# Performance work log

Hardware: AMD Instinct MI355X
Metric: run time of the kernel (lower is better)

Reference implementation:

```python
import jax, jax.numpy as jnp
import numpy as np

B, T, V, E, H, L = 64, 512, 100, 100, 256, 8


def _lstm_layer(xs, w_ih, w_hh, b_ih, b_hh):
    # xs: [B, T, I]; PyTorch gate order: i, f, g, o
    gx = jnp.einsum('bti,gi->btg', xs, w_ih) + b_ih  # [B, T, 4H]
    gx = jnp.swapaxes(gx, 0, 1)                      # [T, B, 4H]
    w_hh_t = w_hh.T                                  # [H, 4H]
    h0 = jnp.zeros((xs.shape[0], w_hh.shape[1]), xs.dtype)

    def step(carry, g):
        h, c = carry
        g = g + h @ w_hh_t + b_hh
        i, f, gg, o = jnp.split(g, 4, axis=-1)
        c = jax.nn.sigmoid(f) * c + jax.nn.sigmoid(i) * jnp.tanh(gg)
        h = jax.nn.sigmoid(o) * jnp.tanh(c)
        return (h, c), h

    (hT, cT), ys = jax.lax.scan(step, (h0, h0), gx)
    return jnp.swapaxes(ys, 0, 1), hT, cT


def setup_inputs() -> dict:
    key = jax.random.key(0)
    ks = jax.random.split(key, 9)
    s = 0.05  # roughly PyTorch's 1/sqrt(H) uniform scale
    return {
        'x': jax.random.randint(ks[0], (B, T), 0, V),
        'embed': jax.random.normal(ks[1], (V, E), jnp.float32) * s,
        'w_ih0': jax.random.normal(ks[2], (4 * H, E), jnp.float32) * s,
        'w_ih': jax.random.normal(ks[3], (L - 1, 4 * H, H), jnp.float32) * s,
        'w_hh': jax.random.normal(ks[4], (L, 4 * H, H), jnp.float32) * s,
        'b_ih': jax.random.normal(ks[5], (L, 4 * H), jnp.float32) * s,
        'b_hh': jax.random.normal(ks[6], (L, 4 * H), jnp.float32) * s,
        'fc_w': jax.random.normal(ks[7], (V, H), jnp.float32) * s,
        'fc_b': jax.random.normal(ks[8], (V,), jnp.float32) * s,
    }


def reference(x, embed, w_ih0, w_ih, w_hh, b_ih, b_hh, fc_w, fc_b):
    h = embed[x]  # [B, T, E]
    h_fin, c_fin = [], []
    for l in range(L):
        wih = w_ih0 if l == 0 else w_ih[l - 1]
        h, hT, cT = _lstm_layer(h, wih, w_hh[l], b_ih[l], b_hh[l])
        h_fin.append(hT)
        c_fin.append(cT)
    logits = jnp.einsum('bth,vh->btv', h, fc_w) + fc_b  # [B, T, V]
    return logits, jnp.stack(h_fin), jnp.stack(c_fin)
```

## Files before the change

### kernel.cpp

```cpp
#include <hip/hip_runtime.h>


typedef _Float16 f16;
typedef f16  f16x8 __attribute__((ext_vector_type(8)));
typedef f16  f16x4 __attribute__((ext_vector_type(4)));
typedef float f32x4 __attribute__((ext_vector_type(4)));
typedef int   i32x4 __attribute__((ext_vector_type(4)));

#define DEV __device__ __forceinline__

constexpr int TT = 512, BB = 64, VV = 100, HH = 256, LL = 8;
constexpr int RING_D = 32;
constexpr int POISON = 0x7C007C00;
constexpr int MAXRETRY = 4096;

constexpr size_t XE_OFF = 0;
constexpr size_t XE_SZ  = (size_t)TT*BB*256*2;
constexpr size_t WP_OFF = XE_OFF + XE_SZ;
constexpr size_t WP_SZ  = (size_t)LL*16*64*512*2;
constexpr size_t BI_OFF = WP_OFF + WP_SZ;
constexpr size_t BI_SZ  = (size_t)LL*16*64*4;
constexpr size_t FW_OFF = BI_OFF + BI_SZ;
constexpr size_t FW_SZ  = (size_t)112*256*2;
constexpr size_t H7_OFF = FW_OFF + FW_SZ;
constexpr size_t H7_SZ  = (size_t)TT*BB*256*2;
constexpr size_t HR_OFF = H7_OFF + H7_SZ;
constexpr size_t HR_SZ  = (size_t)LL*RING_D*BB*256*2;
constexpr size_t XR_OFF = HR_OFF + HR_SZ;
constexpr size_t XR_SZ  = (size_t)7*RING_D*BB*256*2;
constexpr size_t FCF_OFF = XR_OFF + XR_SZ;
constexpr size_t FCF_SZ  = (size_t)7*TT*16;
constexpr size_t XC_OFF  = FCF_OFF + FCF_SZ;
constexpr size_t XC_SZ   = 128;
constexpr int ZERO_DW = (int)((FCF_SZ + XC_SZ) / 4);
constexpr int POIS_TH = (int)((HR_SZ + XR_SZ) / 16);

DEV void ld16_pl (i32x4& d, const void* p){ asm volatile("global_load_dwordx4 %0, %1, off"     : "=v"(d) : "v"(p)); }
DEV void ld16_sc0(i32x4& d, const void* p){ asm volatile("global_load_dwordx4 %0, %1, off sc0" : "=v"(d) : "v"(p)); }
DEV void ld16_sc1(i32x4& d, const void* p){ asm volatile("global_load_dwordx4 %0, %1, off sc1" : "=v"(d) : "v"(p)); }
DEV void st16_sc0(void* p, i32x4 d){ asm volatile("global_store_dwordx4 %0, %1, off sc0" :: "v"(p), "v"(d) : "memory"); }
DEV void st16_sc1(void* p, i32x4 d){ asm volatile("global_store_dwordx4 %0, %1, off sc1" :: "v"(p), "v"(d) : "memory"); }
DEV void stb_sc1(void* p){ unsigned o = 1; asm volatile("global_store_byte %0, %1, off sc1" :: "v"(p), "v"(o) : "memory"); }
DEV void stb_val_sc1(void* p, unsigned v){ asm volatile("global_store_byte %0, %1, off sc1" :: "v"(p), "v"(v) : "memory"); }
DEV void wait_vm0(){ asm volatile("s_waitcnt vmcnt(0)" ::: "memory"); __builtin_amdgcn_sched_barrier(0); }
DEV void wait_vm8(){ asm volatile("s_waitcnt vmcnt(8)" ::: "memory"); __builtin_amdgcn_sched_barrier(0); }

DEV bool chk8(const i32x4* f) {
  int bad = 0;
  #pragma unroll
  for (int i = 0; i < 8; ++i) {
    bad |= (f[i][0] == POISON);
    bad |= (f[i][1] == POISON);
    bad |= (f[i][2] == POISON);
    bad |= (f[i][3] == POISON);
  }
  return __all(bad == 0);
}

DEV bool poll16(const unsigned char* p) {
  for (int it = 0; it < (1 << 16); ++it) {
    i32x4 f;
    asm volatile("global_load_dwordx4 %0, %1, off sc1\n\ts_waitcnt vmcnt(0)"
                 : "=v"(f) : "v"(p) : "memory");
    if ((f[0] & f[1] & f[2] & f[3]) == 0x01010101) return true;
    if (it > 2) __builtin_amdgcn_s_sleep(1);
  }
  return false;
}

DEV bool hs_poll(const unsigned char* p) {
  for (int it = 0; it < (1 << 20); ++it) {
    i32x4 f;
    asm volatile("global_load_dwordx4 %0, %1, off sc1\n\ts_waitcnt vmcnt(0)"
                 : "=v"(f) : "v"(p) : "memory");
    int a = f[0] & f[1] & f[2] & f[3];
    if ((a & 0x10101010) == 0x10101010) {
      int e = (f[0] & 0xFF) * 0x01010101;
      return f[0] == e && f[1] == e && f[2] == e && f[3] == e;
    }
    __builtin_amdgcn_s_sleep(1);
  }
  return false;
}

DEV float sig2(float y)  { return __builtin_amdgcn_rcpf(1.f + __builtin_amdgcn_exp2f(-y)); }
DEV float tanhp(float y) { return 1.f - 2.f * __builtin_amdgcn_rcpf(1.f + __builtin_amdgcn_exp2f(y)); }
constexpr float LOG2E = 1.4426950408889634f;
constexpr float C2LE  = 2.8853900817779268f;
DEV unsigned f16bits(float v) { f16 h = (f16)v; return (unsigned)__builtin_bit_cast(unsigned short, h); }

__global__ void prep_zero(unsigned int* p, int n) {
  int i = blockIdx.x * 256 + threadIdx.x;
  if (i < n) p[i] = 0;
}
__global__ void prep_poison(unsigned int* p) {
  size_t i = ((size_t)blockIdx.x * 256 + threadIdx.x) * 4;
  i32x4 P = {POISON, POISON, POISON, POISON};
  *(i32x4*)(p + i) = P;
}

__global__ void prep_embed(const int* __restrict__ x, const float* __restrict__ em,
                           f16* __restrict__ xe) {
  int g = blockIdx.x * 256 + threadIdx.x;
  int chunk = g & 7, pair = g >> 3;
  int b = pair & 63, t = pair >> 6;
  int idx = x[b * 512 + t];
  const float* er = em + (size_t)idx * 100;
  f16* o = xe + (size_t)pair * 256 + chunk * 32;
  #pragma unroll
  for (int c4 = 0; c4 < 32; c4 += 4) {
    f16x4 v;
    #pragma unroll
    for (int q = 0; q < 4; ++q) {
      int c = chunk * 32 + c4 + q;
      v[q] = (c < 100) ? (f16)er[c] : (f16)0.f;
    }
    *(f16x4*)(o + c4) = v;
  }
}

__global__ void prep_w(const float* __restrict__ w_ih0, const float* __restrict__ w_ih,
                       const float* __restrict__ w_hh, f16* __restrict__ wpo) {
  int g = blockIdx.x * 256 + threadIdx.x;
  int k4 = (g & 127) * 4;
  int n  = (g >> 7) & 63;
  int ls = g >> 13;
  int l = ls >> 4, s = ls & 15;
  int gate = n & 3;
  int u = s * 16 + ((n >> 4) << 2) + ((n >> 2) & 3);
  int r = 256 * gate + u;
  float scale = (gate == 2) ? C2LE : LOG2E;
  f16x4 v;
  #pragma unroll
  for (int q = 0; q < 4; ++q) {
    int k = k4 + q;
    float f;
    if (k < 256) {
      if (l == 0) f = (k < 100) ? w_ih0[(size_t)r * 100 + k] : 0.f;
      else        f = w_ih[((size_t)(l - 1) * 1024 + r) * 256 + k];
    } else        f = w_hh[((size_t)l * 1024 + r) * 256 + (k - 256)];
    v[q] = (f16)(f * scale);
  }
  *(f16x4*)(wpo + (size_t)g * 4) = v;
}

__global__ void prep_bias(const float* __restrict__ b_ih, const float* __restrict__ b_hh,
                          float* __restrict__ bo) {
  int g = blockIdx.x * 256 + threadIdx.x;
  int n = g & 63, s = (g >> 6) & 15, l = g >> 10;
  int gate = n & 3;
  int u = s * 16 + ((n >> 4) << 2) + ((n >> 2) & 3);
  int r = 256 * gate + u;
  float scale = (gate == 2) ? C2LE : LOG2E;
  bo[g] = (b_ih[l * 1024 + r] + b_hh[l * 1024 + r]) * scale;
}

__global__ void prep_fcw(const float* __restrict__ fc_w, f16* __restrict__ fo) {
  int g = blockIdx.x * 256 + threadIdx.x;
  int n = g >> 6, k4 = (g & 63) * 4;
  f16x4 v;
  #pragma unroll
  for (int q = 0; q < 4; ++q)
    v[q] = (n < 100) ? (f16)fc_w[(size_t)n * 256 + k4 + q] : (f16)0.f;
  *(f16x4*)(fo + (size_t)g * 4) = v;
}

__global__ void __launch_bounds__(512, 1) lstm_pipe(
    const f16* __restrict__ xe, const f16* __restrict__ wp, const float* __restrict__ biasp,
    f16* h7, f16* hrg, f16* xrg, unsigned char* fcf, unsigned char* xc, float* out)
{
  __shared__ char pad_lds[40960];
  __shared__ unsigned short pub[2][64][24];
  (void)((volatile char*)pad_lds)[threadIdx.x];

  const int bx  = blockIdx.x;
  const int lyr = bx & 7;
  const int sl  = bx >> 3;
  const int tid = threadIdx.x;
  const int wv  = tid >> 6;
  const int ln  = tid & 63;
  const int mA  = wv >> 2;
  const int nB  = wv & 3;

  f16x8 wfa[2][16];
  {
    const f16* wb = wp + (size_t)(lyr * 16 + sl) * 64 * 512;
    #pragma unroll
    for (int tt = 0; tt < 2; ++tt)
      #pragma unroll
      for (int kt = 0; kt < 16; ++kt) {
        wfa[tt][kt] = *(const f16x8*)(wb + (size_t)((2 * mA + tt) * 16 + (ln & 15)) * 512
                                      + kt * 32 + (ln >> 4) * 8);
        i32x4 pin = __builtin_bit_cast(i32x4, wfa[tt][kt]);
        asm volatile("" : "+v"(pin));
        wfa[tt][kt] = __builtin_bit_cast(f16x8, pin);
      }
  }
  f32x4 bias_v[2];
  #pragma unroll
  for (int tt = 0; tt < 2; ++tt) {
    bias_v[tt] = *(const f32x4*)(biasp + (size_t)(lyr * 16 + sl) * 64
                                 + (2 * mA + tt) * 16 + (ln >> 4) * 4);
    asm volatile("" : "+v"(bias_v[tt]));
  }

  unsigned xcc = 0;
  asm volatile("s_getreg_b32 %0, hwreg(20, 0, 32)" : "=s"(xcc));
  unsigned char* xcg = xc + lyr * 16;
  if (tid == 0) stb_val_sc1(xcg + sl, 0x10 | (xcc & 15));
  const bool fast = hs_poll(xcg);

  float cst0 = 0.f, cst1 = 0.f;
  const int q    = ln >> 4;
  const int bcol = nB * 16 + (ln & 15);
  const int kof  = q * 8;
  const f16* xring = xrg + (size_t)(lyr - 1) * RING_D * 16384;
  f16*       xdst  = xrg + (size_t)lyr * RING_D * 16384;
  f16*       hring = hrg + (size_t)lyr * RING_D * 16384;
  bool dead = false;

  for (int t = 0; t < TT; ++t) {
    if (wv == 0 && t + 1 < TT) {
      if (lyr < 7 && t + 1 >= RING_D && !dead)
        dead = !poll16(fcf + (size_t)(lyr * TT + (t + 1 - RING_D)) * 16);
      i32x4 P = {POISON, POISON, POISON, POISON};
      f16* pz = hring + (size_t)((t + 1) & (RING_D - 1)) * 16384
              + (size_t)ln * 256 + sl * 16;
      if (fast) { st16_sc0(pz, P); st16_sc0(pz + 8, P); }
      else      { st16_sc1(pz, P); st16_sc1(pz + 8, P); }
      if (lyr < 7) {
        f16* px = xdst + (size_t)((t + 1) & (RING_D - 1)) * 16384
                + (size_t)ln * 256 + sl * 16;
        st16_sc1(px, P);
        st16_sc1(px + 8, P);
      }
    }

    const bool hasH = (t > 0);
    i32x4 bfx[8], bfh[8];
    {
      const f16* xb = ((lyr == 0) ? xe + (size_t)t * 16384
                                  : xring + (size_t)(t & (RING_D - 1)) * 16384)
                      + (size_t)bcol * 256 + kof;
      if (lyr == 0) {
        #pragma unroll
        for (int kt = 0; kt < 8; ++kt) ld16_pl(bfx[kt], xb + kt * 32);
      } else {
        #pragma unroll
        for (int kt = 0; kt < 8; ++kt) ld16_sc1(bfx[kt], xb + kt * 32);
      }
      if (hasH) {
        const f16* hb = hring + (size_t)((t - 1) & (RING_D - 1)) * 16384
                      + (size_t)bcol * 256 + kof;
        if (fast) {
          #pragma unroll
          for (int kt = 0; kt < 8; ++kt) ld16_sc0(bfh[kt], hb + kt * 32);
        } else {
          #pragma unroll
          for (int kt = 0; kt < 8; ++kt) ld16_sc1(bfh[kt], hb + kt * 32);
        }
      }
    }
    if (hasH) wait_vm8(); else wait_vm0();

    if (lyr > 0 && !dead) {
      int it = 0;
      while (!chk8(bfx)) {
        if (++it > MAXRETRY) { dead = true; break; }
        wait_vm0();
        const f16* xb = xring + (size_t)(t & (RING_D - 1)) * 16384
                      + (size_t)bcol * 256 + kof;
        #pragma unroll
        for (int kt = 0; kt < 8; ++kt) ld16_sc1(bfx[kt], xb + kt * 32);
        wait_vm0();
      }
    }

    f32x4 acc0 = {0,0,0,0}, acc1 = {0,0,0,0};
    #pragma unroll
    for (int kt = 0; kt < 8; ++kt) {
      f16x8 av = __builtin_bit_cast(f16x8, bfx[kt]);
      acc0 = __builtin_amdgcn_mfma_f32_16x16x32_f16(wfa[0][kt], av, acc0, 0, 0, 0);
      acc1 = __builtin_amdgcn_mfma_f32_16x16x32_f16(wfa[1][kt], av, acc1, 0, 0, 0);
    }

    if (hasH) {
      wait_vm0();
      if (!dead) {
        int it = 0;
        while (!chk8(bfh)) {
          if (++it > MAXRETRY) { dead = true; break; }
          const f16* hb = hring + (size_t)((t - 1) & (RING_D - 1)) * 16384
                        + (size_t)bcol * 256 + kof;
          if (fast) {
            #pragma unroll
            for (int kt = 0; kt < 8; ++kt) ld16_sc0(bfh[kt], hb + kt * 32);
          } else {
            #pragma unroll
            for (int kt = 0; kt < 8; ++kt) ld16_sc1(bfh[kt], hb + kt * 32);
          }
          wait_vm0();
        }
      }
      #pragma unroll
      for (int kt = 0; kt < 8; ++kt) {
        f16x8 av = __builtin_bit_cast(f16x8, bfh[kt]);
        acc0 = __builtin_amdgcn_mfma_f32_16x16x32_f16(wfa[0][8 + kt], av, acc0, 0, 0, 0);
        acc1 = __builtin_amdgcn_mfma_f32_16x16x32_f16(wfa[1][8 + kt], av, acc1, 0, 0, 0);
      }
    }

    const int par = t & 1;
    #pragma unroll
    for (int tt = 0; tt < 2; ++tt) {
      f32x4 g4 = (tt == 0 ? acc0 : acc1);
      g4 += bias_v[tt];
      float i_ = sig2(g4[0]), f_ = sig2(g4[1]), z_ = tanhp(g4[2]), o_ = sig2(g4[3]);
      float& c_ = (tt == 0 ? cst0 : cst1);
      c_ = f_ * c_ + i_ * z_;
      float h_ = o_ * tanhp(c_ * C2LE);
      pub[par][bcol][(2 * mA + tt) * 4 + q] = (unsigned short)f16bits(h_);
      if (t == TT - 1) {
        const int u = sl * 16 + (2 * mA + tt) * 4 + q;
        size_t ob = 3276800 + (size_t)lyr * 16384 + (size_t)bcol * 256 + u;
        out[ob] = h_;  out[ob + 131072] = c_;
      }
    }
    __syncthreads();

    if (wv == 0) {
      i32x4 d0 = *(const i32x4*)&pub[par][ln][0];
      i32x4 d1 = *(const i32x4*)&pub[par][ln][8];
      f16* hd = hring + (size_t)(t & (RING_D - 1)) * 16384 + (size_t)ln * 256 + sl * 16;
      if (fast) { st16_sc0(hd, d0); st16_sc0(hd + 8, d1); }
      else      { st16_sc1(hd, d0); st16_sc1(hd + 8, d1); }
      if (lyr < 7) {
        f16* xd = xdst + (size_t)(t & (RING_D - 1)) * 16384 + (size_t)ln * 256 + sl * 16;
        st16_sc1(xd, d0);
        st16_sc1(xd + 8, d1);
      } else {
        f16* h7d = h7 + (size_t)t * 16384 + (size_t)ln * 256 + sl * 16;
        *(i32x4*)h7d = d0;
        *(i32x4*)(h7d + 8) = d1;
      }
      if (ln == 1 && lyr > 0)
        stb_sc1(fcf + (size_t)((lyr - 1) * TT + t) * 16 + sl);
    }
  }
}

__global__ void __launch_bounds__(256, 1) fc_kernel(
    const f16* __restrict__ h7, const f16* __restrict__ fcw,
    const float* __restrict__ fcb, float* __restrict__ out)
{
  const int t  = blockIdx.x;
  const int wv = threadIdx.x >> 6;
  const int ln = threadIdx.x & 63;
  const f16* ab = h7 + (size_t)t * 16384 + (size_t)(wv * 16 + (ln & 15)) * 256 + (ln >> 4) * 8;
  f16x8 af[8];
  #pragma unroll
  for (int kt = 0; kt < 8; ++kt) af[kt] = *(const f16x8*)(ab + kt * 32);
  const int obrow = wv * 16 + (ln >> 4) * 4;
  #pragma unroll
  for (int nt = 0; nt < 7; ++nt) {
    const f16* bb = fcw + (size_t)(nt * 16 + (ln & 15)) * 256 + (ln >> 4) * 8;
    f32x4 acc = {0, 0, 0, 0};
    #pragma unroll
    for (int kt = 0; kt < 8; ++kt) {
      f16x8 bv = *(const f16x8*)(bb + kt * 32);
      acc = __builtin_amdgcn_mfma_f32_16x16x32_f16(af[kt], bv, acc, 0, 0, 0);
    }
    int vg = nt * 16 + (ln & 15);
    if (vg < VV) {
      float bias = fcb[vg];
      #pragma unroll
      for (int j = 0; j < 4; ++j)
        out[(size_t)(obrow + j) * 51200 + (size_t)t * 100 + vg] = acc[j] + bias;
    }
  }
}

extern "C" void kernel_launch(void* const* d_in, const int* in_sizes, int n_in,
                              void* d_out, int out_size, void* d_ws, size_t ws_size,
                              hipStream_t stream) {
  (void)in_sizes; (void)n_in; (void)out_size; (void)ws_size;
  const int*   x     = (const int*)d_in[0];
  const float* embed = (const float*)d_in[1];
  const float* w_ih0 = (const float*)d_in[2];
  const float* w_ih  = (const float*)d_in[3];
  const float* w_hh  = (const float*)d_in[4];
  const float* b_ih  = (const float*)d_in[5];
  const float* b_hh  = (const float*)d_in[6];
  const float* fc_w  = (const float*)d_in[7];
  const float* fc_b  = (const float*)d_in[8];
  char* ws = (char*)d_ws;
  float* out = (float*)d_out;

  prep_zero<<<57, 256, 0, stream>>>((unsigned int*)(ws + FCF_OFF), ZERO_DW);
  prep_poison<<<POIS_TH / 256, 256, 0, stream>>>((unsigned int*)(ws + HR_OFF));
  prep_embed<<<1024, 256, 0, stream>>>(x, embed, (f16*)(ws + XE_OFF));
  prep_w<<<4096, 256, 0, stream>>>(w_ih0, w_ih, w_hh, (f16*)(ws + WP_OFF));
  prep_bias<<<32, 256, 0, stream>>>(b_ih, b_hh, (float*)(ws + BI_OFF));
  prep_fcw<<<28, 256, 0, stream>>>(fc_w, (f16*)(ws + FW_OFF));

  lstm_pipe<<<128, 512, 35072, stream>>>(
      (const f16*)(ws + XE_OFF), (const f16*)(ws + WP_OFF), (const float*)(ws + BI_OFF),
      (f16*)(ws + H7_OFF), (f16*)(ws + HR_OFF), (f16*)(ws + XR_OFF),
      (unsigned char*)(ws + FCF_OFF), (unsigned char*)(ws + XC_OFF), out);

  fc_kernel<<<512, 256, 0, stream>>>((const f16*)(ws + H7_OFF), (const f16*)(ws + FW_OFF),
                                     fc_b, out);
}
```

Before: 3.215 ms.

## Software-pipeline input projection one timestep ahead of recurrent step in LSTM pipe

```diff
diff --git a/kernel.cpp b/kernel.cpp
--- a/kernel.cpp
+++ b/kernel.cpp
@@ -33,7 +33,7 @@
 constexpr size_t XC_OFF  = FCF_OFF + FCF_SZ;
 constexpr size_t XC_SZ   = 128;
 constexpr int ZERO_DW = (int)((FCF_SZ + XC_SZ) / 4);
-constexpr int POIS_TH = (int)((HR_SZ + XR_SZ) / 16);
+constexpr int POIS_BLK = (int)((HR_SZ + XR_SZ) / 16 / 256);
 
 DEV void ld16_pl (i32x4& d, const void* p){ asm volatile("global_load_dwordx4 %0, %1, off"     : "=v"(d) : "v"(p)); }
 DEV void ld16_sc0(i32x4& d, const void* p){ asm volatile("global_load_dwordx4 %0, %1, off sc0" : "=v"(d) : "v"(p)); }
@@ -219,73 +219,55 @@
   f16*       hring = hrg + (size_t)lyr * RING_D * 16384;
   bool dead = false;
 
-  for (int t = 0; t < TT; ++t) {
-    if (wv == 0 && t + 1 < TT) {
-      if (lyr < 7 && t + 1 >= RING_D && !dead)
-        dead = !poll16(fcf + (size_t)(lyr * TT + (t + 1 - RING_D)) * 16);
-      i32x4 P = {POISON, POISON, POISON, POISON};
-      f16* pz = hring + (size_t)((t + 1) & (RING_D - 1)) * 16384
-              + (size_t)ln * 256 + sl * 16;
-      if (fast) { st16_sc0(pz, P); st16_sc0(pz + 8, P); }
-      else      { st16_sc1(pz, P); st16_sc1(pz + 8, P); }
-      if (lyr < 7) {
-        f16* px = xdst + (size_t)((t + 1) & (RING_D - 1)) * 16384
-                + (size_t)ln * 256 + sl * 16;
-        st16_sc1(px, P);
-        st16_sc1(px + 8, P);
-      }
-    }
-
-    const bool hasH = (t > 0);
-    i32x4 bfx[8], bfh[8];
-    {
-      const f16* xb = ((lyr == 0) ? xe + (size_t)t * 16384
-                                  : xring + (size_t)(t & (RING_D - 1)) * 16384)
-                      + (size_t)bcol * 256 + kof;
-      if (lyr == 0) {
-        #pragma unroll
-        for (int kt = 0; kt < 8; ++kt) ld16_pl(bfx[kt], xb + kt * 32);
-      } else {
-        #pragma unroll
-        for (int kt = 0; kt < 8; ++kt) ld16_sc1(bfx[kt], xb + kt * 32);
-      }
-      if (hasH) {
-        const f16* hb = hring + (size_t)((t - 1) & (RING_D - 1)) * 16384
-                      + (size_t)bcol * 256 + kof;
-        if (fast) {
-          #pragma unroll
-          for (int kt = 0; kt < 8; ++kt) ld16_sc0(bfh[kt], hb + kt * 32);
-        } else {
-          #pragma unroll
-          for (int kt = 0; kt < 8; ++kt) ld16_sc1(bfh[kt], hb + kt * 32);
-        }
-      }
-    }
-    if (hasH) wait_vm8(); else wait_vm0();
-
-    if (lyr > 0 && !dead) {
+  i32x4 bfx[8], bfh[8];
+  f32x4 aX0 = {0,0,0,0}, aX1 = {0,0,0,0};
+
+  {
+    const f16* xb = ((lyr == 0) ? xe : xring) + (size_t)bcol * 256 + kof;
+    if (lyr == 0) { 
+      #pragma unroll
+      for (int kt = 0; kt < 8; ++kt) ld16_pl(bfx[kt], xb + kt * 32);
+    } else {
+      #pragma unroll
+      for (int kt = 0; kt < 8; ++kt) ld16_sc1(bfx[kt], xb + kt * 32);
+    }
+    wait_vm0();
+    if (lyr > 0) {
       int it = 0;
       while (!chk8(bfx)) {
         if (++it > MAXRETRY) { dead = true; break; }
-        wait_vm0();
-        const f16* xb = xring + (size_t)(t & (RING_D - 1)) * 16384
-                      + (size_t)bcol * 256 + kof;
         #pragma unroll
         for (int kt = 0; kt < 8; ++kt) ld16_sc1(bfx[kt], xb + kt * 32);
         wait_vm0();
       }
     }
-
-    f32x4 acc0 = {0,0,0,0}, acc1 = {0,0,0,0};
     #pragma unroll
     for (int kt = 0; kt < 8; ++kt) {
       f16x8 av = __builtin_bit_cast(f16x8, bfx[kt]);
-      acc0 = __builtin_amdgcn_mfma_f32_16x16x32_f16(wfa[0][kt], av, acc0, 0, 0, 0);
-      acc1 = __builtin_amdgcn_mfma_f32_16x16x32_f16(wfa[1][kt], av, acc1, 0, 0, 0);
-    }
-
+      aX0 = __builtin_amdgcn_mfma_f32_16x16x32_f16(wfa[0][kt], av, aX0, 0, 0, 0);
+      aX1 = __builtin_amdgcn_mfma_f32_16x16x32_f16(wfa[1][kt], av, aX1, 0, 0, 0);
+    }
+    if (lyr > 0 && wv == 0 && ln == 1)
+      stb_sc1(fcf + (size_t)((lyr - 1) * TT + 0) * 16 + sl);
+    const f16* xb1 = ((lyr == 0) ? xe + 16384 : xring + 16384)
+                     + (size_t)bcol * 256 + kof;
+    if (lyr == 0) {
+      #pragma unroll
+      for (int kt = 0; kt < 8; ++kt) ld16_pl(bfx[kt], xb1 + kt * 32);
+    } else {
+      #pragma unroll
+      for (int kt = 0; kt < 8; ++kt) ld16_sc1(bfx[kt], xb1 + kt * 32);
+    }
+  }
+
+  for (int t = 0; t < TT; ++t) {
+    const bool hasH  = (t > 0);
+    const bool lastT = (t == TT - 1);
+
+    wait_vm8();
+
+    f32x4 a0 = aX0, a1 = aX1;
     if (hasH) {
-      wait_vm0();
       if (!dead) {
         int it = 0;
         while (!chk8(bfh)) {
@@ -305,25 +287,67 @@
       #pragma unroll
       for (int kt = 0; kt < 8; ++kt) {
         f16x8 av = __builtin_bit_cast(f16x8, bfh[kt]);
-        acc0 = __builtin_amdgcn_mfma_f32_16x16x32_f16(wfa[0][8 + kt], av, acc0, 0, 0, 0);
-        acc1 = __builtin_amdgcn_mfma_f32_16x16x32_f16(wfa[1][8 + kt], av, acc1, 0, 0, 0);
+        a0 = __builtin_amdgcn_mfma_f32_16x16x32_f16(wfa[0][8 + kt], av, a0, 0, 0, 0);
+        a1 = __builtin_amdgcn_mfma_f32_16x16x32_f16(wfa[1][8 + kt], av, a1, 0, 0, 0);
+      }
+    }
+
+    if (!lastT) {
+      wait_vm0();
+      if (lyr > 0 && !dead) {
+        int it = 0;
+        while (!chk8(bfx)) {
+          if (++it > MAXRETRY) { dead = true; break; }
+          const f16* xb = xring + (size_t)((t + 1) & (RING_D - 1)) * 16384
+                        + (size_t)bcol * 256 + kof;
+          #pragma unroll
+          for (int kt = 0; kt < 8; ++kt) ld16_sc1(bfx[kt], xb + kt * 32);
+          wait_vm0();
+        }
+      }
+      aX0 = f32x4{0,0,0,0}; aX1 = f32x4{0,0,0,0};
+      #pragma unroll
+      for (int kt = 0; kt < 8; ++kt) {
+        f16x8 av = __builtin_bit_cast(f16x8, bfx[kt]);
+        aX0 = __builtin_amdgcn_mfma_f32_16x16x32_f16(wfa[0][kt], av, aX0, 0, 0, 0);
+        aX1 = __builtin_amdgcn_mfma_f32_16x16x32_f16(wfa[1][kt], av, aX1, 0, 0, 0);
       }
     }
 
     const int par = t & 1;
     #pragma unroll
     for (int tt = 0; tt < 2; ++tt) {
-      f32x4 g4 = (tt == 0 ? acc0 : acc1);
+      f32x4 g4 = (tt == 0 ? a0 : a1);
       g4 += bias_v[tt];
       float i_ = sig2(g4[0]), f_ = sig2(g4[1]), z_ = tanhp(g4[2]), o_ = sig2(g4[3]);
       float& c_ = (tt == 0 ? cst0 : cst1);
       c_ = f_ * c_ + i_ * z_;
       float h_ = o_ * tanhp(c_ * C2LE);
       pub[par][bcol][(2 * mA + tt) * 4 + q] = (unsigned short)f16bits(h_);
-      if (t == TT - 1) {
+      if (lastT) {
         const int u = sl * 16 + (2 * mA + tt) * 4 + q;
         size_t ob = 3276800 + (size_t)lyr * 16384 + (size_t)bcol * 256 + u;
         out[ob] = h_;  out[ob + 131072] = c_;
+      }
+    }
+
+    if (wv == 0) {
+      if (lyr > 0 && !lastT && ln == 1)
+        stb_sc1(fcf + (size_t)((lyr - 1) * TT + (t + 1)) * 16 + sl);
+      if (t + 2 < TT) {
+        if (lyr < 7 && t >= 30 && !dead)
+          dead = !poll16(fcf + (size_t)(lyr * TT + (t - 30)) * 16);
+        i32x4 P = {POISON, POISON, POISON, POISON};
+        f16* pz = hring + (size_t)((t + 2) & (RING_D - 1)) * 16384
+                + (size_t)ln * 256 + sl * 16;
+        if (fast) { st16_sc0(pz, P); st16_sc0(pz + 8, P); }
+        else      { st16_sc1(pz, P); st16_sc1(pz + 8, P); }
+        if (lyr < 7) {
+          f16* px = xdst + (size_t)((t + 2) & (RING_D - 1)) * 16384
+                  + (size_t)ln * 256 + sl * 16;
+          st16_sc1(px, P);
+          st16_sc1(px + 8, P);
+        }
       }
     }
     __syncthreads();
@@ -343,8 +367,28 @@
         *(i32x4*)h7d = d0;
         *(i32x4*)(h7d + 8) = d1;
       }
-      if (ln == 1 && lyr > 0)
-        stb_sc1(fcf + (size_t)((lyr - 1) * TT + t) * 16 + sl);
+    }
+    if (!lastT) {
+      const f16* hb = hring + (size_t)(t & (RING_D - 1)) * 16384
+                    + (size_t)bcol * 256 + kof;
+      if (fast) {
+        #pragma unroll
+        for (int kt = 0; kt < 8; ++kt) ld16_sc0(bfh[kt], hb + kt * 32);
+      } else {
+        #pragma unroll
+        for (int kt = 0; kt < 8; ++kt) ld16_sc1(bfh[kt], hb + kt * 32);
+      }
+      int tx = (t + 2 < TT) ? (t + 2) : (TT - 1);
+      const f16* xb = ((lyr == 0) ? xe + (size_t)tx * 16384
+                                  : xring + (size_t)(tx & (RING_D - 1)) * 16384)
+                      + (size_t)bcol * 256 + kof;
+      if (lyr == 0) {
+        #pragma unroll
+        for (int kt = 0; kt < 8; ++kt) ld16_pl(bfx[kt], xb + kt * 32);
+      } else {
+        #pragma unroll
+        for (int kt = 0; kt < 8; ++kt) ld16_sc1(bfx[kt], xb + kt * 32);
+      }
     }
   }
 }
@@ -396,8 +440,8 @@
   char* ws = (char*)d_ws;
   float* out = (float*)d_out;
 
-  prep_zero<<<57, 256, 0, stream>>>((unsigned int*)(ws + FCF_OFF), ZERO_DW);
-  prep_poison<<<POIS_TH / 256, 256, 0, stream>>>((unsigned int*)(ws + HR_OFF));
+  prep_zero<<<(ZERO_DW + 255) / 256, 256, 0, stream>>>((unsigned int*)(ws + FCF_OFF), ZERO_DW);
+  prep_poison<<<POIS_BLK, 256, 0, stream>>>((unsigned int*)(ws + HR_OFF));
   prep_embed<<<1024, 256, 0, stream>>>(x, embed, (f16*)(ws + XE_OFF));
   prep_w<<<4096, 256, 0, stream>>>(w_ih0, w_ih, w_hh, (f16*)(ws + WP_OFF));
   prep_bias<<<32, 256, 0, stream>>>(b_ih, b_hh, (float*)(ws + BI_OFF));
```

New measurement: 3.541 ms. 1.1x slower.
